# Kernel optimization log

Hardware: AMD Instinct MI355X
Metric: run time of the kernel (lower is better)

Reference implementation:

```python
import jax, jax.numpy as jnp
import numpy as np

B, P, J, MOT, K, NB, WN, H = 64, 12273, 80, 94, 64, 20, 17, 128
W_POSE = 1.0

def euler_to_rotmat(a):
    # a: [..., 3] radians, R = Rz @ Ry @ Rx
    sx, sy, sz = jnp.sin(a[..., 0]), jnp.sin(a[..., 1]), jnp.sin(a[..., 2])
    cx, cy, cz = jnp.cos(a[..., 0]), jnp.cos(a[..., 1]), jnp.cos(a[..., 2])
    r00 = cz * cy; r01 = cz * sy * sx - sz * cx; r02 = cz * sy * cx + sz * sx
    r10 = sz * cy; r11 = sz * sy * sx + cz * cx; r12 = sz * sy * cx - cz * sx
    r20 = -sy;     r21 = cy * sx;                r22 = cy * cx
    return jnp.stack([jnp.stack([r00, r01, r02], -1),
                      jnp.stack([r10, r11, r12], -1),
                      jnp.stack([r20, r21, r22], -1)], -2)

def setup_inputs() -> dict:
    key = jax.random.key(0)
    ks = jax.random.split(key, 20)
    f32 = jnp.float32
    return {
        'in_pc_batch': jax.random.normal(ks[0], (B, P, 3), f32),
        't_nor': jax.random.normal(ks[1], (B, P, 3), f32),
        'rest_verts': jax.random.normal(ks[2], (P, 3), f32),
        'skin_weights': jax.random.uniform(ks[3], (P, J), f32),
        'mul_weight_list': jax.random.normal(ks[4], (J, MOT), f32),
        'query': jax.random.normal(ks[5], (B, J, 3), f32),
        'cloth_pose_std': jax.random.uniform(ks[6], (3,), f32),
        'cloth_pose_mean': jax.random.normal(ks[7], (3,), f32),
        'cloth_trans_std': jax.random.uniform(ks[8], (3,), f32),
        'cloth_trans_mean': jax.random.normal(ks[9], (3,), f32),
        'W1': jax.random.normal(ks[10], (3 + K, H), f32) * 0.1,
        'b1': jnp.zeros((H,), f32),
        'W2': jax.random.normal(ks[11], (H, 6), f32) * 0.1,
        'b2': jnp.zeros((6,), f32),
        'tmtemp': jax.random.normal(ks[12], (B, MOT, K), f32),
        'Wd': jax.random.normal(ks[13], (MOT * K, NB * WN), f32) * 0.02,
        'bd': jnp.zeros((NB * WN,), f32),
        'DPSD': jax.random.normal(ks[14], (NB, WN, P, 3), f32) * 0.1,
        'ssdr_res_std': jax.random.uniform(ks[15], (3,), f32),
        'ssdr_res_mean': jax.random.normal(ks[16], (3,), f32),
    }

def reference(in_pc_batch, t_nor, rest_verts, skin_weights, mul_weight_list,
              query, cloth_pose_std, cloth_pose_mean, cloth_trans_std,
              cloth_trans_mean, W1, b1, W2, b2, tmtemp, Wd, bd, DPSD,
              ssdr_res_std, ssdr_res_mean):
    # per-joint field input: [B, J, K]
    field_input = jnp.einsum('bjk,lj->blk', tmtemp, jax.nn.relu(mul_weight_list))
    # FieldNet: per-joint MLP on concat(query, field_input) -> [B, J, 6]
    h = jnp.concatenate([query, field_input], axis=-1)
    pred_rt = jax.nn.relu(h @ W1 + b1) @ W2 + b2
    pred_pose = pred_rt[..., 0:3] * cloth_pose_std + cloth_pose_mean
    pred_trans = (query + pred_rt[..., 3:6]) * cloth_trans_std + cloth_trans_mean
    # detailsnet + fused 20-basis accumulation: [B, P, 3]
    nbat = tmtemp.shape[0]
    detailkey = (tmtemp.reshape(nbat, -1) @ Wd + bd).reshape(nbat, NB, WN)
    detail_res = jnp.einsum('bnw,nwpx->bpx', detailkey, DPSD)
    detail_res = detail_res * ssdr_res_std + ssdr_res_mean
    # SSDR LBS skinning with Euler-angle rotations (degrees -> radians)
    R = euler_to_rotmat(jnp.deg2rad(pred_pose))            # [B, J, 3, 3]
    skinned = (jnp.einsum('pj,bjxy,py->bpx', skin_weights, R, rest_verts)
               + jnp.einsum('pj,bjx->bpx', skin_weights, pred_trans))
    out_pc = skinned + detail_res                          # [B, P, 3]
    loss_pose_l1 = jnp.mean(jnp.abs(in_pc_batch[:, :, 0:3] - out_pc))
    loss = loss_pose_l1 * W_POSE + 1e-4 * jnp.mean(DPSD ** 2)
    return loss[None], out_pc
```

## Files before the change

### kernel.cpp

```cpp
#include <hip/hip_runtime.h>

#define B_   64
#define P_   12273
#define J_   80
#define MOT_ 94
#define K_   64
#define H_   128
#define Q_   340
#define NE_  36819
#define MK_  6016
#define PW_  12288

typedef float v4f  __attribute__((ext_vector_type(4)));
typedef float v8f  __attribute__((ext_vector_type(8)));
typedef float v16f __attribute__((ext_vector_type(16)));
#define AS4 __attribute__((address_space(4)))

__device__ __forceinline__ const AS4 float* unif(const float* p){
  return (const AS4 float*)(unsigned long long)p;
}
__device__ __forceinline__ const AS4 v4f* univ4(const float* p){
  return (const AS4 v4f*)(unsigned long long)p;
}
__device__ __forceinline__ const AS4 v8f* univ8(const float* p){
  return (const AS4 v8f*)(unsigned long long)p;
}
__device__ __forceinline__ const AS4 v16f* univ16(const float* p){
  return (const AS4 v16f*)(unsigned long long)p;
}

__global__ __launch_bounds__(256) void k_prep(
    const float* __restrict__ query, const float* __restrict__ mwl,
    const float* __restrict__ tm,    const float* __restrict__ W1,
    const float* __restrict__ b1,    const float* __restrict__ W2,
    const float* __restrict__ b2,    const float* __restrict__ cps,
    const float* __restrict__ cpm,   const float* __restrict__ cts,
    const float* __restrict__ ctm,   const float* __restrict__ skin,
    float* __restrict__ G,           float* __restrict__ tm_t,
    float* __restrict__ w_t,         float* __restrict__ lacc)
{
  __shared__ float smem[80 * 65];
  int blk = blockIdx.x;
  int t = threadIdx.x;
  if (blk < 1280){
    int lane = t & 63;
    int wid = __builtin_amdgcn_readfirstlane(t >> 6);
    int bj = blk * 4 + wid;
    int b = bj / J_, l = bj - b * J_;
    float* hs = smem + wid * 80;
    float acc = 0.f;
    const AS4 float* mp = unif(mwl + l * MOT_);
    const float* tp = tm + (size_t)b * MK_ + lane;
    #pragma unroll 2
    for (int j = 0; j < MOT_; j++){
      float w = mp[j]; w = w > 0.f ? w : 0.f;
      acc = fmaf(w, tp[j * K_], acc);
    }
    hs[3 + lane] = acc;
    if (lane < 3) hs[lane] = query[(size_t)bj * 3 + lane];
    __syncthreads();
    float a1 = b1[lane], a2 = b1[lane + 64];
    for (int i = 0; i < 3 + K_; i++){
      float hv = hs[i];
      a1 = fmaf(hv, W1[i * H_ + lane], a1);
      a2 = fmaf(hv, W1[i * H_ + 64 + lane], a2);
    }
    a1 = a1 > 0.f ? a1 : 0.f;
    a2 = a2 > 0.f ? a2 : 0.f;
    const AS4 float* b2c = unif(b2);
    float rt[6];
    #pragma unroll
    for (int o = 0; o < 6; o++){
      float po = fmaf(a1, W2[lane * 6 + o], a2 * W2[(lane + 64) * 6 + o]);
      #pragma unroll
      for (int off = 32; off; off >>= 1) po += __shfl_xor(po, off);
      rt[o] = po + b2c[o];
    }
    const float D2R = 0.017453292519943295f;
    float ax = fmaf(rt[0], cps[0], cpm[0]) * D2R;
    float ay = fmaf(rt[1], cps[1], cpm[1]) * D2R;
    float az = fmaf(rt[2], cps[2], cpm[2]) * D2R;
    float tx = fmaf(hs[0] + rt[3], cts[0], ctm[0]);
    float ty = fmaf(hs[1] + rt[4], cts[1], ctm[1]);
    float tz = fmaf(hs[2] + rt[5], cts[2], ctm[2]);
    float sx, cx, sy, cy, sz, cz;
    sincosf(ax, &sx, &cx); sincosf(ay, &sy, &cy); sincosf(az, &sz, &cz);
    if (lane == 0){
      float4 r0 = make_float4(cz*cy, cz*sy*sx - sz*cx, cz*sy*cx + sz*sx, tx);
      float4 r1 = make_float4(sz*cy, sz*sy*sx + cz*cx, sz*sy*cx - cz*sx, ty);
      float4 r2 = make_float4(-sy,   cy*sx,            cy*cx,            tz);
      float4* g = (float4*)(G + (size_t)bj * 12);
      g[0] = r0; g[1] = r1; g[2] = r2;
    }
  } else if (blk < 1374){
    int m0 = (blk - 1280) * 64;
    int ml = t & 63, g = t >> 6;
    #pragma unroll
    for (int r = 0; r < 16; r++){
      int b = g * 16 + r;
      smem[ml * 65 + b] = tm[(size_t)b * MK_ + m0 + ml];
    }
    __syncthreads();
    int bl = t & 63;
    #pragma unroll
    for (int r = 0; r < 16; r++){
      int m = g * 16 + r;
      tm_t[(size_t)(m0 + m) * 64 + bl] = smem[m * 65 + bl];
    }
  } else if (blk < 1566){
    int p0 = (blk - 1374) * 64;
    #pragma unroll
    for (int k = 0; k < 20; k++){
      int idx = k * 256 + t;
      int pl = idx / 80, j = idx - pl * 80;
      int p = p0 + pl;
      smem[j * 65 + pl] = (p < P_) ? skin[(size_t)p * J_ + j] : 0.f;
    }
    __syncthreads();
    #pragma unroll
    for (int k = 0; k < 20; k++){
      int idx = k * 256 + t;
      int j = idx >> 6, pl = idx & 63;
      w_t[(size_t)j * PW_ + p0 + pl] = smem[j * 65 + pl];
    }
  } else {
    if (t < 2) lacc[t] = 0.f;
  }
}

__global__ __launch_bounds__(256) void k_dkey(
    const float* __restrict__ tm_t, const float* __restrict__ Wd,
    float* __restrict__ part)
{
  int t = threadIdx.x;
  int lane = t & 63;
  int wid = __builtin_amdgcn_readfirstlane(t >> 6);
  int qt = blockIdx.x;
  int q = qt * 64 + lane;
  bool vq = q < Q_;
  int m0 = blockIdx.y * 64;
  const AS4 v16f* tr = univ16(tm_t);
  float acc[16];
  #pragma unroll
  for (int i = 0; i < 16; i++) acc[i] = 0.f;
  float wbuf[4];
  #pragma unroll
  for (int i = 0; i < 4; i++)
    wbuf[i] = vq ? Wd[(size_t)(m0 + i) * Q_ + q] : 0.f;
  v16f tb0 = tr[(size_t)(m0 + 0) * 4 + wid];
  v16f tb1 = tr[(size_t)(m0 + 1) * 4 + wid];
  #pragma unroll 4
  for (int mm = 0; mm < 60; mm++){
    float wd = wbuf[mm & 3];
    wbuf[mm & 3] = vq ? Wd[(size_t)(m0 + mm + 4) * Q_ + q] : 0.f;
    v16f tv = tb0; tb0 = tb1;
    tb1 = tr[(size_t)(m0 + mm + 2) * 4 + wid];
    #pragma unroll
    for (int i = 0; i < 16; i++) acc[i] = fmaf(tv[i], wd, acc[i]);
  }
  #pragma unroll
  for (int mm = 60; mm < 64; mm++){
    float wd = wbuf[mm & 3];
    v16f tv = tb0; tb0 = tb1;
    if (mm < 62) tb1 = tr[(size_t)(m0 + mm + 2) * 4 + wid];
    #pragma unroll
    for (int i = 0; i < 16; i++) acc[i] = fmaf(tv[i], wd, acc[i]);
  }
  float* pb = part + ((size_t)blockIdx.y * 6 + qt) * 4096 + (size_t)(wid * 16) * 64;
  #pragma unroll
  for (int i = 0; i < 16; i++) pb[i * 64 + lane] = acc[i];
}

__global__ __launch_bounds__(256) void k_dkred(
    const float* __restrict__ part, const float* __restrict__ bd,
    float* __restrict__ dk_t, int S)
{
  int t = threadIdx.x;
  int jj = blockIdx.x * 32 + (t >> 3);
  int dl = t & 7;
  int b = jj / Q_, q = jj - b * Q_;
  int qt = q >> 6, ql = q & 63;
  const float* pp = part + (size_t)qt * 4096 + b * 64 + ql;
  float s = 0.f;
  for (int d = dl; d < S; d += 8) s += pp[(size_t)d * 6 * 4096];
  s += __shfl_xor(s, 1); s += __shfl_xor(s, 2); s += __shfl_xor(s, 4);
  if (dl == 0) dk_t[q * 64 + b] = bd[q] + s;
}

__global__ __launch_bounds__(512) void k_detail(
    const float* __restrict__ DPSD, const float* __restrict__ dk_t,
    float* __restrict__ stg0, float* __restrict__ out,
    float* __restrict__ lacc, int qn)
{
  int t = threadIdx.x;
  int lane = t & 63;
  int wid = __builtin_amdgcn_readfirstlane(t >> 6);
  int b0 = wid * 8;
  int e = blockIdx.x * 64 + lane;
  bool ve = e < NE_;
  int q0 = blockIdx.y * qn;
  const AS4 v8f* dkv = univ8(dk_t + b0);
  const float* Dp = DPSD + e;
  float acc[8];
  #pragma unroll
  for (int i = 0; i < 8; i++) acc[i] = 0.f;
  float sq = 0.f;
  float dc[5], dn[5];
  #pragma unroll
  for (int i = 0; i < 5; i++)
    dc[i] = ve ? Dp[(size_t)(q0 + i) * NE_] : 0.f;
  int ng = qn / 5;
  for (int g = 0; g < ng; g++){
    int qq = q0 + g * 5;
    if (g + 1 < ng){
      #pragma unroll
      for (int i = 0; i < 5; i++)
        dn[i] = ve ? Dp[(size_t)(qq + 5 + i) * NE_] : 0.f;
    }
    v8f r0 = dkv[(qq + 0) * 8];
    v8f r1 = dkv[(qq + 1) * 8];
    v8f r2 = dkv[(qq + 2) * 8];
    v8f r3 = dkv[(qq + 3) * 8];
    v8f r4 = dkv[(qq + 4) * 8];
    if (wid == 0){
      #pragma unroll
      for (int i = 0; i < 5; i++) sq = fmaf(dc[i], dc[i], sq);
    }
    #pragma unroll
    for (int i = 0; i < 8; i++){
      acc[i] = fmaf(r0[i], dc[0], acc[i]);
      acc[i] = fmaf(r1[i], dc[1], acc[i]);
      acc[i] = fmaf(r2[i], dc[2], acc[i]);
      acc[i] = fmaf(r3[i], dc[3], acc[i]);
      acc[i] = fmaf(r4[i], dc[4], acc[i]);
    }
    #pragma unroll
    for (int i = 0; i < 5; i++) dc[i] = dn[i];
  }
  if (ve){
    bool toOut = (blockIdx.y + 1 == gridDim.y);
    float* dst = toOut ? (out + 1 + e) : (stg0 + e);
    #pragma unroll
    for (int i = 0; i < 8; i++)
      dst[(size_t)(b0 + i) * NE_] = acc[i];
  }
  if (wid == 0){
    #pragma unroll
    for (int off = 32; off; off >>= 1) sq += __shfl_xor(sq, off);
    if (lane == 0) atomicAdd(&lacc[1], sq);
  }
}

__global__ __launch_bounds__(256) void k_skin(
    const float* __restrict__ G, const float* __restrict__ w_t,
    const float* __restrict__ rest, const float* __restrict__ in_pc,
    const float* __restrict__ stg0, const float* __restrict__ rstd,
    const float* __restrict__ rmean,
    float* __restrict__ out, float* __restrict__ lacc, int two)
{
  int t = threadIdx.x;
  int lane = t & 63;
  int wid = __builtin_amdgcn_readfirstlane(t >> 6);
  int p  = blockIdx.x * 64 + lane;
  int bA = blockIdx.y * 8 + wid * 2;
  const AS4 v4f* gA = univ4(G + (size_t)bA * J_ * 12);
  const AS4 v4f* gB = univ4(G + ((size_t)bA + 1) * J_ * 12);
  float accA[12], accB[12];
  #pragma unroll
  for (int c = 0; c < 12; c++){ accA[c] = 0.f; accB[c] = 0.f; }
  const float* wp = w_t + p;
  #pragma unroll 4
  for (int j = 0; j < J_; j++){
    float w = wp[(size_t)j * PW_];
    v4f a0 = gA[j * 3 + 0], a1 = gA[j * 3 + 1], a2 = gA[j * 3 + 2];
    v4f c0 = gB[j * 3 + 0], c1 = gB[j * 3 + 1], c2 = gB[j * 3 + 2];
    #pragma unroll
    for (int c = 0; c < 4; c++){
      accA[c]     = fmaf(w, a0[c], accA[c]);
      accA[4 + c] = fmaf(w, a1[c], accA[4 + c]);
      accA[8 + c] = fmaf(w, a2[c], accA[8 + c]);
      accB[c]     = fmaf(w, c0[c], accB[c]);
      accB[4 + c] = fmaf(w, c1[c], accB[4 + c]);
      accB[8 + c] = fmaf(w, c2[c], accB[8 + c]);
    }
  }
  bool vp = p < P_;
  float vx = 0.f, vy = 0.f, vz = 0.f;
  if (vp){ vx = rest[p * 3]; vy = rest[p * 3 + 1]; vz = rest[p * 3 + 2]; }
  float srs[3], srm[3];
  #pragma unroll
  for (int x = 0; x < 3; x++){ srs[x] = rstd[x]; srm[x] = rmean[x]; }
  float lsum = 0.f;
  if (vp){
    size_t baseA = ((size_t)bA * P_ + p) * 3;
    size_t baseB = baseA + (size_t)P_ * 3;
    #pragma unroll
    for (int x = 0; x < 3; x++){
      float det = out[1 + baseA + x];
      if (two) det += stg0[baseA + x];
      float v = fmaf(accA[x*4+0], vx, fmaf(accA[x*4+1], vy, fmaf(accA[x*4+2], vz, accA[x*4+3])));
      v += fmaf(det, srs[x], srm[x]);
      lsum += fabsf(in_pc[baseA + x] - v);
      out[1 + baseA + x] = v;
    }
    #pragma unroll
    for (int x = 0; x < 3; x++){
      float det = out[1 + baseB + x];
      if (two) det += stg0[baseB + x];
      float v = fmaf(accB[x*4+0], vx, fmaf(accB[x*4+1], vy, fmaf(accB[x*4+2], vz, accB[x*4+3])));
      v += fmaf(det, srs[x], srm[x]);
      lsum += fabsf(in_pc[baseB + x] - v);
      out[1 + baseB + x] = v;
    }
  }
  #pragma unroll
  for (int off = 32; off; off >>= 1) lsum += __shfl_xor(lsum, off);
  __shared__ float red[4];
  if (lane == 0) red[wid] = lsum;
  __syncthreads();
  if (t == 0) atomicAdd(&lacc[0], red[0] + red[1] + red[2] + red[3]);
}

__global__ void k_finalize(const float* __restrict__ lacc, float* __restrict__ out){
  if (threadIdx.x == 0 && blockIdx.x == 0){
    float loss = lacc[0] * (1.f / 2356416.f) + 1e-4f * (lacc[1] * (1.f / 12518460.f));
    out[0] = loss;
  }
}

extern "C" void kernel_launch(void* const* d_in, const int* in_sizes, int n_in,
                              void* d_out, int out_size, void* d_ws, size_t ws_size,
                              hipStream_t stream){
  const float* in_pc = (const float*)d_in[0];
  const float* rest  = (const float*)d_in[2];
  const float* skin  = (const float*)d_in[3];
  const float* mwl   = (const float*)d_in[4];
  const float* query = (const float*)d_in[5];
  const float* cps   = (const float*)d_in[6];
  const float* cpm   = (const float*)d_in[7];
  const float* cts   = (const float*)d_in[8];
  const float* ctm   = (const float*)d_in[9];
  const float* W1    = (const float*)d_in[10];
  const float* b1    = (const float*)d_in[11];
  const float* W2    = (const float*)d_in[12];
  const float* b2    = (const float*)d_in[13];
  const float* tm    = (const float*)d_in[14];
  const float* Wd    = (const float*)d_in[15];
  const float* bd    = (const float*)d_in[16];
  const float* DPSD  = (const float*)d_in[17];
  const float* rstd  = (const float*)d_in[18];
  const float* rmean = (const float*)d_in[19];
  float* out = (float*)d_out;

  float* ws   = (float*)d_ws;
  float* G    = ws;
  float* dk_t = G + 61440;
  float* lacc = dk_t + 21760;
  float* tm_t = lacc + 64;
  float* w_t  = tm_t + 385024;
  float* un   = w_t + 983040;

  size_t have = ws_size / 4;
  int nqh = (have >= (size_t)(1451328 + 2356416)) ? 2 : 1;
  int qn = Q_ / nqh;

  k_prep    <<<1567, 256, 0, stream>>>(query, mwl, tm, W1, b1, W2, b2,
                                       cps, cpm, cts, ctm, skin,
                                       G, tm_t, w_t, lacc);
  k_dkey    <<<dim3(6, 94), 256, 0, stream>>>(tm_t, Wd, un);
  k_dkred   <<<680, 256, 0, stream>>>(un, bd, dk_t, 94);
  k_detail  <<<dim3(576, nqh), 512, 0, stream>>>(DPSD, dk_t, un, out, lacc, qn);
  k_skin    <<<dim3(192, 8), 256, 0, stream>>>(G, w_t, rest, in_pc, un, rstd, rmean,
                                               out, lacc, nqh - 1);
  k_finalize<<<1, 64, 0, stream>>>(lacc, out);
}
```

Baseline: 272.4 us.

## Widen detail kernel to 16 batches per wave with two-deep DPSD prefetch

The detail basis-accumulation kernel now uses 4 waves of 256 threads, each covering 16 batch columns instead of 8, so every DPSD element loaded is reused across twice as many batches. The main loop is unrolled by two groups and keeps two groups of DPSD loads in flight, and out-of-range lanes clamp their address instead of doing predicated loads. The cost is more accumulator registers and lower occupancy. The final two groups are handled outside the loop, which assumes qn/5 is at least 2.

Result: faster. 255.5 us (-6.2%).

```diff
diff --git a/kernel.cpp b/kernel.cpp
--- a/kernel.cpp
+++ b/kernel.cpp
@@ -187,7 +187,30 @@
   if (dl == 0) dk_t[q * 64 + b] = bd[q] + s;
 }
 
-__global__ __launch_bounds__(512) void k_detail(
+__device__ __forceinline__ void dconsume(const AS4 v16f* dkv, int qa, int wid,
+                                         const float* dc, float* acc,
+                                         float& sq, bool doSq)
+{
+  v16f r0 = dkv[(qa + 0) * 4 + wid];
+  v16f r1 = dkv[(qa + 1) * 4 + wid];
+  v16f r2 = dkv[(qa + 2) * 4 + wid];
+  v16f r3 = dkv[(qa + 3) * 4 + wid];
+  v16f r4 = dkv[(qa + 4) * 4 + wid];
+  if (doSq){
+    #pragma unroll
+    for (int i = 0; i < 5; i++) sq = fmaf(dc[i], dc[i], sq);
+  }
+  #pragma unroll
+  for (int i = 0; i < 16; i++){
+    acc[i] = fmaf(r0[i], dc[0], acc[i]);
+    acc[i] = fmaf(r1[i], dc[1], acc[i]);
+    acc[i] = fmaf(r2[i], dc[2], acc[i]);
+    acc[i] = fmaf(r3[i], dc[3], acc[i]);
+    acc[i] = fmaf(r4[i], dc[4], acc[i]);
+  }
+}
+
+__global__ __launch_bounds__(256) void k_detail(
     const float* __restrict__ DPSD, const float* __restrict__ dk_t,
     float* __restrict__ stg0, float* __restrict__ out,
     float* __restrict__ lacc, int qn)
@@ -195,56 +218,49 @@
   int t = threadIdx.x;
   int lane = t & 63;
   int wid = __builtin_amdgcn_readfirstlane(t >> 6);
-  int b0 = wid * 8;
+  int b0 = wid * 16;
   int e = blockIdx.x * 64 + lane;
   bool ve = e < NE_;
   int q0 = blockIdx.y * qn;
-  const AS4 v8f* dkv = univ8(dk_t + b0);
-  const float* Dp = DPSD + e;
-  float acc[8];
-  #pragma unroll
-  for (int i = 0; i < 8; i++) acc[i] = 0.f;
+  const AS4 v16f* dkv = univ16(dk_t);
+  const float* Dp = DPSD + (ve ? e : 0);
+  float acc[16];
+  #pragma unroll
+  for (int i = 0; i < 16; i++) acc[i] = 0.f;
   float sq = 0.f;
-  float dc[5], dn[5];
-  #pragma unroll
-  for (int i = 0; i < 5; i++)
-    dc[i] = ve ? Dp[(size_t)(q0 + i) * NE_] : 0.f;
+  bool doSq = (wid == 0);
+  float da[5], db[5];
+  #pragma unroll
+  for (int i = 0; i < 5; i++) da[i] = Dp[(size_t)(q0 + i) * NE_];
+  #pragma unroll
+  for (int i = 0; i < 5; i++) db[i] = Dp[(size_t)(q0 + 5 + i) * NE_];
   int ng = qn / 5;
-  for (int g = 0; g < ng; g++){
-    int qq = q0 + g * 5;
-    if (g + 1 < ng){
-      #pragma unroll
-      for (int i = 0; i < 5; i++)
-        dn[i] = ve ? Dp[(size_t)(qq + 5 + i) * NE_] : 0.f;
-    }
-    v8f r0 = dkv[(qq + 0) * 8];
-    v8f r1 = dkv[(qq + 1) * 8];
-    v8f r2 = dkv[(qq + 2) * 8];
-    v8f r3 = dkv[(qq + 3) * 8];
-    v8f r4 = dkv[(qq + 4) * 8];
-    if (wid == 0){
-      #pragma unroll
-      for (int i = 0; i < 5; i++) sq = fmaf(dc[i], dc[i], sq);
-    }
-    #pragma unroll
-    for (int i = 0; i < 8; i++){
-      acc[i] = fmaf(r0[i], dc[0], acc[i]);
-      acc[i] = fmaf(r1[i], dc[1], acc[i]);
-      acc[i] = fmaf(r2[i], dc[2], acc[i]);
-      acc[i] = fmaf(r3[i], dc[3], acc[i]);
-      acc[i] = fmaf(r4[i], dc[4], acc[i]);
-    }
-    #pragma unroll
-    for (int i = 0; i < 5; i++) dc[i] = dn[i];
-  }
+  int g = 0;
+  for (; g + 2 < ng; g += 2){
+    int qa = q0 + g * 5;
+    float ta[5], tb[5];
+    #pragma unroll
+    for (int i = 0; i < 5; i++) ta[i] = Dp[(size_t)(qa + 10 + i) * NE_];
+    dconsume(dkv, qa, wid, da, acc, sq, doSq);
+    #pragma unroll
+    for (int i = 0; i < 5; i++) da[i] = ta[i];
+    #pragma unroll
+    for (int i = 0; i < 5; i++) tb[i] = Dp[(size_t)(qa + 15 + i) * NE_];
+    dconsume(dkv, qa + 5, wid, db, acc, sq, doSq);
+    #pragma unroll
+    for (int i = 0; i < 5; i++) db[i] = tb[i];
+  }
+  dconsume(dkv, q0 + (ng - 2) * 5, wid, da, acc, sq, doSq);
+  dconsume(dkv, q0 + (ng - 1) * 5, wid, db, acc, sq, doSq);
   if (ve){
     bool toOut = (blockIdx.y + 1 == gridDim.y);
     float* dst = toOut ? (out + 1 + e) : (stg0 + e);
     #pragma unroll
-    for (int i = 0; i < 8; i++)
+    for (int i = 0; i < 16; i++)
       dst[(size_t)(b0 + i) * NE_] = acc[i];
   }
-  if (wid == 0){
+  if (doSq){
+    if (!ve) sq = 0.f;
     #pragma unroll
     for (int off = 32; off; off >>= 1) sq += __shfl_xor(sq, off);
     if (lane == 0) atomicAdd(&lacc[1], sq);
@@ -369,7 +385,7 @@
                                        G, tm_t, w_t, lacc);
   k_dkey    <<<dim3(6, 94), 256, 0, stream>>>(tm_t, Wd, un);
   k_dkred   <<<680, 256, 0, stream>>>(un, bd, dk_t, 94);
-  k_detail  <<<dim3(576, nqh), 512, 0, stream>>>(DPSD, dk_t, un, out, lacc, qn);
+  k_detail  <<<dim3(576, nqh), 256, 0, stream>>>(DPSD, dk_t, un, out, lacc, qn);
   k_skin    <<<dim3(192, 8), 256, 0, stream>>>(G, w_t, rest, in_pc, un, rstd, rmean,
                                                out, lacc, nqh - 1);
   k_finalize<<<1, 64, 0, stream>>>(lacc, out);
```
